# Kernel tuning notes

Hardware: AMD Instinct MI355X
Metric: run time of the kernel (lower is better)

## Reference

```python
import jax, jax.numpy as jnp
import numpy as np
from jax import lax

EPS = 1e-4
DN = ('NDHWC', 'DHWIO', 'NDHWC')


def _m(mask, dtype):
    return mask[..., None].astype(dtype)


def bn_relu(x, mask):
    # BatchNorm1d over active voxels only (training-mode batch stats, gamma=1, beta=0), then ReLU.
    m = _m(mask, x.dtype)
    n = jnp.sum(m)
    mean = jnp.sum(x * m, axis=(0, 1, 2, 3)) / n
    xc = (x - mean) * m  # re-mask: inactive voxels stay exactly zero
    var = jnp.sum(xc * xc, axis=(0, 1, 2, 3)) / n
    return jnp.maximum(xc * lax.rsqrt(var + EPS), 0.0)


def subm3(x, w, mask):
    # SubMConv3d k=3 pad=1: dense conv on zero-at-inactive input, output restricted to active sites.
    y = lax.conv_general_dilated(x, w, (1, 1, 1), 'SAME', dimension_numbers=DN)
    return y * _m(mask, x.dtype)


def down2(x, w):
    # SparseConv3d k=2 s=2: non-overlapping windows; inactive inputs are zero so dense strided conv matches.
    return lax.conv_general_dilated(x, w, (2, 2, 2), 'VALID', dimension_numbers=DN)


def pool_mask(mask):
    B, D, H, W = mask.shape
    return jnp.any(mask.reshape(B, D // 2, 2, H // 2, 2, W // 2, 2), axis=(2, 4, 6))


def up2(x, w, mask):
    # SparseInverseConv3d k=2 (indice_key inverse of the stride-2 conv): conv-transpose masked to original indices.
    y = jnp.einsum('bdhwc,ijkco->bdihjwko', x, w)
    B, Dc, _, Hc, _, Wc, _, Co = y.shape
    return y.reshape(B, 2 * Dc, 2 * Hc, 2 * Wc, Co) * _m(mask, x.dtype)


def resblock(x, mask, wa, wb, w_sc=None):
    # ResidualBlock: i_branch (identity or 1x1 Custom1x1Subm3d: feats @ W.T) + BN-ReLU-SubM-BN-ReLU-SubM.
    idb = x if w_sc is None else jnp.einsum('bdhwc,oc->bdhwo', x, w_sc)
    h = bn_relu(x, mask)
    h = subm3(h, wa, mask)
    h = bn_relu(h, mask)
    h = subm3(h, wb, mask)
    return h + idb


def unet_forward(x, mask, w_in, w_b1a, w_b1b, w_d1, w_b2a, w_b2b, w_d2,
                 w_b3a, w_b3b, w_u2, w_t2_sc, w_t2a, w_t2b, w_u1, w_t1_sc, w_t1a, w_t1b):
    mask2 = pool_mask(mask)
    mask3 = pool_mask(mask2)
    x0 = subm3(x, w_in, mask)                 # input_conv (subm1)
    x1 = resblock(x0, mask, w_b1a, w_b1b)     # level-1 block (32->32)
    d1 = down2(bn_relu(x1, mask), w_d1)       # BN-ReLU + stride-2 conv 32->64
    x2 = resblock(d1, mask2, w_b2a, w_b2b)    # level-2 block (64->64)
    d2 = down2(bn_relu(x2, mask2), w_d2)      # 64->96
    x3 = resblock(d2, mask3, w_b3a, w_b3b)    # bottom level (96->96)
    u2 = up2(bn_relu(x3, mask3), w_u2, mask2)  # BN-ReLU + inverse conv 96->64
    t2 = resblock(jnp.concatenate([x2, u2], -1), mask2, w_t2a, w_t2b, w_t2_sc)  # tail 128->64
    u1 = up2(bn_relu(t2, mask2), w_u1, mask)   # 64->32
    t1 = resblock(jnp.concatenate([x1, u1], -1), mask, w_t1a, w_t1b, w_t1_sc)   # tail 64->32
    return bn_relu(t1, mask)                   # output_layer: BN + ReLU


def setup_inputs() -> dict:
    key = jax.random.key(0)
    ks = jax.random.split(key, 20)
    B, D = 1, 48
    Cin, C1, C2, C3 = 6, 32, 64, 96
    mask = jax.random.uniform(ks[0], (B, D, D, D)) < 0.12
    x = jax.random.normal(ks[1], (B, D, D, D, Cin), jnp.float32) * mask[..., None]

    def w(k, shape):
        fan = float(np.prod(shape[:-1]))
        return (jax.random.normal(k, shape, jnp.float32) / np.sqrt(fan)).astype(jnp.float32)

    return {
        'x': x, 'mask': mask,
        'w_in': w(ks[2], (3, 3, 3, Cin, C1)),
        'w_b1a': w(ks[3], (3, 3, 3, C1, C1)), 'w_b1b': w(ks[4], (3, 3, 3, C1, C1)),
        'w_d1': w(ks[5], (2, 2, 2, C1, C2)),
        'w_b2a': w(ks[6], (3, 3, 3, C2, C2)), 'w_b2b': w(ks[7], (3, 3, 3, C2, C2)),
        'w_d2': w(ks[8], (2, 2, 2, C2, C3)),
        'w_b3a': w(ks[9], (3, 3, 3, C3, C3)), 'w_b3b': w(ks[10], (3, 3, 3, C3, C3)),
        'w_u2': w(ks[11], (2, 2, 2, C3, C2)),
        'w_t2_sc': w(ks[12], (C2, 2 * C2)),
        'w_t2a': w(ks[13], (3, 3, 3, 2 * C2, C2)), 'w_t2b': w(ks[14], (3, 3, 3, C2, C2)),
        'w_u1': w(ks[15], (2, 2, 2, C2, C1)),
        'w_t1_sc': w(ks[16], (C1, 2 * C1)),
        'w_t1a': w(ks[17], (3, 3, 3, 2 * C1, C1)), 'w_t1b': w(ks[18], (3, 3, 3, C1, C1)),
    }


def reference(x, mask, w_in, w_b1a, w_b1b, w_d1, w_b2a, w_b2b, w_d2,
              w_b3a, w_b3b, w_u2, w_t2_sc, w_t2a, w_t2b, w_u1, w_t1_sc, w_t1a, w_t1b):
    return unet_forward(x, mask, w_in, w_b1a, w_b1b, w_d1, w_b2a, w_b2b, w_d2,
                        w_b3a, w_b3b, w_u2, w_t2_sc, w_t2a, w_t2b, w_u1, w_t1_sc, w_t1a, w_t1b)
```

## Files before the change

### kernel.cpp

```cpp
#include <hip/hip_runtime.h>


typedef short bf16x8 __attribute__((ext_vector_type(8)));
typedef float f32x4 __attribute__((ext_vector_type(4)));
typedef unsigned short ushort_t;

constexpr int D1 = 48, DIM2 = 24, DIM3 = 12;
constexpr int N1 = D1 * D1 * D1;
constexpr int N2 = DIM2 * DIM2 * DIM2;
constexpr int N3 = DIM3 * DIM3 * DIM3;

constexpr size_t OFF_A      = 0;
constexpr size_t OFF_R1     = 3538944;
constexpr size_t OFF_CAT1   = 7077888;
constexpr size_t OFF_D1R    = 14155776;
constexpr size_t OFF_R3     = 15040512;
constexpr size_t OFF_CAT2   = 15925248;
constexpr size_t OFF_D2R    = 17694720;
constexpr size_t OFF_R4     = 17860608;
constexpr size_t OFF_X3R    = 18026496;
constexpr size_t OFF_BN1_32 = 18192384;
constexpr size_t OFF_BN1_64 = 19961920;
constexpr size_t OFF_BN2_64 = 23500928;
constexpr size_t OFF_BN2_128= 23943360;
constexpr size_t OFF_BN3_96 = 24828160;
constexpr size_t OFF_BFEND  = 24911168;
constexpr size_t OFF_WT     = 24911168;
constexpr size_t OFF_STATS  = 25634112;
constexpr size_t STATS_FLOATS = 15 * 2048 * 2;
constexpr size_t OFF_CNT    = OFF_STATS + STATS_FLOATS;
constexpr size_t OFF_L1     = OFF_CNT + 16;
constexpr size_t OFF_L2     = OFF_L1 + N1;
constexpr size_t OFF_L3     = OFF_L2 + N2;
constexpr size_t OFF_M1     = OFF_L3 + N3;
constexpr size_t OFF_M2     = OFF_M1 + N1 / 4;
constexpr size_t OFF_M3     = OFF_M2 + N2 / 4;

constexpr int WTS[16] = {0, 32768, 65536, 98304, 114688, 229376, 344064,
                         393216, 669696, 946176, 1175552, 1290240, 1347584,
                         1380352, 1429504, 1445888};

__device__ inline ushort_t f2bf(float f) {
  union { float f; unsigned u; } x; x.f = f;
  unsigned u = x.u + 0x7FFF + ((x.u >> 16) & 1);
  return (ushort_t)(u >> 16);
}

__global__ __launch_bounds__(256) void k_mask1(const float* __restrict__ x,
                                               unsigned char* __restrict__ m,
                                               int* __restrict__ list, int* __restrict__ cnt) {
  int v = blockIdx.x * 256 + threadIdx.x;
  if (v >= N1) return;
  const float* p = x + (size_t)v * 6;
  bool a = (p[0] != 0.f) || (p[1] != 0.f) || (p[2] != 0.f) ||
           (p[3] != 0.f) || (p[4] != 0.f) || (p[5] != 0.f);
  m[v] = a ? 1 : 0;
  if (a) { int pos = atomicAdd(cnt, 1); list[pos] = v; }
}

__global__ __launch_bounds__(256) void k_pool(const unsigned char* __restrict__ mf,
                                              unsigned char* __restrict__ mc,
                                              int* __restrict__ list, int* __restrict__ cnt, int DC) {
  int v = blockIdx.x * 256 + threadIdx.x;
  int n = DC * DC * DC;
  if (v >= n) return;
  int w = v % DC, h = (v / DC) % DC, d = v / (DC * DC);
  int DF = 2 * DC;
  bool a = false;
  for (int i = 0; i < 2; i++)
    for (int j = 0; j < 2; j++)
      for (int k = 0; k < 2; k++)
        a |= (mf[(size_t)(((2 * d + i) * DF + (2 * h + j)) * DF + (2 * w + k))] != 0);
  mc[v] = a ? 1 : 0;
  if (a) { int pos = atomicAdd(cnt, 1); list[pos] = v; }
}

struct WJobs {
  const float* src[15];
  int start[16];
  short cinr[15], cipad[15], cout[15], kk[15];
};

__global__ __launch_bounds__(256) void k_wprep(WJobs jb, ushort_t* __restrict__ wt, int total) {
  int gid = blockIdx.x * 256 + threadIdx.x;
  if (gid >= total) return;
  int j = 0;
#pragma unroll
  for (int jj = 0; jj < 15; jj++)
    if (gid >= jb.start[jj + 1]) j = jj + 1;
  int e = gid - jb.start[j];
  int CIP = jb.cipad[j], CO = jb.cout[j], CIR = jb.cinr[j], KKr = jb.kk[j];
  int ci = e % CIP;
  int co = (e / CIP) % CO;
  int k = e / (CIP * CO);
  float v = (k < KKr && ci < CIR) ? jb.src[j][((size_t)k * CIR + ci) * CO + co] : 0.f;
  wt[gid] = f2bf(v);
}

__global__ __launch_bounds__(256) void k_xprep(const float* __restrict__ x, ushort_t* __restrict__ xp) {
  int gid = blockIdx.x * 256 + threadIdx.x;
  if (gid >= (N1 + 4) * 8) return;
  int v = gid >> 3, c = (gid & 7) * 4;
  uint2 o = make_uint2(0u, 0u);
  if (v < N1) {
    ushort_t u[4];
#pragma unroll
    for (int j = 0; j < 4; j++) {
      int ci = c + j;
      float f = (ci < 6) ? x[(size_t)v * 6 + ci] : 0.f;
      u[j] = f2bf(f);
    }
    o.x = (unsigned)u[0] | ((unsigned)u[1] << 16);
    o.y = (unsigned)u[2] | ((unsigned)u[3] << 16);
  }
  *(uint2*)&xp[(size_t)v * 32 + c] = o;
}

template <int CIPAD, int COUT, int KK, bool UP>
__global__ __launch_bounds__(512, 2) void k_conv4(
    const ushort_t* __restrict__ in, const ushort_t* __restrict__ wt,
    float* __restrict__ out, int ostride, int ooff,
    const float* __restrict__ res, int rstride,
    double* __restrict__ st,
    const int* __restrict__ list, const int* __restrict__ cnt, int DD) {
  constexpr int KCH = CIPAD / 32;
  constexpr int UNITS = KK * KCH;
  constexpr int KPW = (UNITS + 7) / 8;
  __shared__ float red[8][8][64];
  __shared__ float fin[16][33];
  __shared__ int vidx[16];

  int n = cnt[0];
  int base = blockIdx.x * 16;
  if (base >= n) return;
  int t = threadIdx.x, wv = t >> 6, ln = t & 63;
  int fr = ln & 15, kg = ln >> 4;
  int coblk = blockIdx.y * 32;
  if (t < 16) vidx[t] = (base + t < n) ? list[base + t] : -1;

  int ai = base + fr;
  int av = (ai < n) ? list[ai] : -1;
  int vv = av < 0 ? 0 : av;
  int ad = vv / (DD * DD), ah = (vv / DD) % DD, aw = vv % DD;
  int pidx = 0, corner = 0;
  if (UP) {
    int DC = DD / 2;
    pidx = (((ad >> 1) * DC) + (ah >> 1)) * DC + (aw >> 1);
    corner = ((ad & 1) << 2) | ((ah & 1) << 1) | (aw & 1);
  }
  const int GDI = UP ? (DD >> 1) : ((KK == 8) ? 2 * DD : DD);
  const int SENT = GDI * GDI * GDI;

  f32x4 acc0 = (f32x4){0.f, 0.f, 0.f, 0.f};
  f32x4 acc1 = (f32x4){0.f, 0.f, 0.f, 0.f};

  bf16x8 aR[KPW], b0R[KPW], b1R[KPW];
#pragma unroll
  for (int i = 0; i < KPW; i++) {
    int u = wv + i * 8;
    int k = u / KCH, c = u - k * KCH;
    int kc = (k < KK) ? k : KK - 1;
    int nix;
    if (UP) {
      nix = (av >= 0 && corner == kc) ? pidx : SENT;
    } else if (KK == 27) {
      int kd = kc / 9 - 1, kh = (kc / 3) % 3 - 1, kw = kc % 3 - 1;
      int nd = ad + kd, nh = ah + kh, nw = aw + kw;
      bool inb = (av >= 0) && (unsigned)nd < (unsigned)DD &&
                 (unsigned)nh < (unsigned)DD && (unsigned)nw < (unsigned)DD;
      nix = inb ? (nd * DD + nh) * DD + nw : SENT;
    } else {
      nix = (av >= 0) ? ((2 * ad + ((kc >> 2) & 1)) * GDI + (2 * ah + ((kc >> 1) & 1))) * GDI +
                        (2 * aw + (kc & 1))
                      : SENT;
    }
    aR[i] = *(const bf16x8*)(in + (size_t)nix * CIPAD + c * 32 + kg * 8);
    const ushort_t* wb = wt + ((size_t)(k * COUT + coblk + fr)) * CIPAD + c * 32 + kg * 8;
    b0R[i] = *(const bf16x8*)wb;
    b1R[i] = *(const bf16x8*)(wb + (size_t)16 * CIPAD);
  }
#pragma unroll
  for (int i = 0; i < KPW; i++) {
    acc0 = __builtin_amdgcn_mfma_f32_16x16x32_bf16(aR[i], b0R[i], acc0, 0, 0, 0);
    acc1 = __builtin_amdgcn_mfma_f32_16x16x32_bf16(aR[i], b1R[i], acc1, 0, 0, 0);
  }

#pragma unroll
  for (int r = 0; r < 4; r++) {
    red[wv][r][ln] = acc0[r];
    red[wv][4 + r][ln] = acc1[r];
  }
  __syncthreads();
  {
    int e = t >> 6, l = t & 63;
    float s = 0.f;
#pragma unroll
    for (int w = 0; w < 8; w++) s += red[w][e][l];
    int f = e >> 2, r = e & 3;
    int fr2 = l & 15, kg2 = l >> 4;
    int slot = kg2 * 4 + r;
    int co = f * 16 + fr2;
    int v = vidx[slot];
    float val = 0.f;
    if (v >= 0) {
      int gco = coblk + co;
      val = s;
      if (res) val += res[(size_t)v * rstride + gco];
      out[(size_t)v * ostride + ooff + gco] = val;
    }
    fin[slot][co] = val;
  }
  __syncthreads();
  if (t < 32) {
    float sm = 0.f, sq = 0.f;
#pragma unroll
    for (int p = 0; p < 16; p++) {
      float x = fin[p][t];
      sm += x; sq += x * x;
    }
    double* sr = st + (size_t)(blockIdx.x & 7) * 256;
    atomicAdd(&sr[coblk + t], (double)sm);
    atomicAdd(&sr[128 + coblk + t], (double)sq);
  }
}

template <int C>
__global__ __launch_bounds__(256) void k_bnapply2(
    const float* __restrict__ x, int xstr,
    const double* __restrict__ sA, const double* __restrict__ sB, int csplit,
    const int* __restrict__ list, const int* __restrict__ cnt,
    ushort_t* __restrict__ out) {
  __shared__ float mu_s[C], inv_s[C];
  int n = cnt[0];
  int t = threadIdx.x;
  if (t < C) {
    const double* s = (t < csplit) ? (sA + t) : (sB + (t - csplit));
    double sm = 0.0, sq = 0.0;
#pragma unroll
    for (int r = 0; r < 8; r++) { sm += s[r * 256]; sq += s[r * 256 + 128]; }
    double mu = sm / n;
    double var = sq / n - mu * mu;
    mu_s[t] = (float)mu;
    inv_s[t] = rsqrtf((float)fmax(var, 0.0) + 1e-4f);
  }
  __syncthreads();
  int total = n * (C / 4);
  for (int gid = blockIdx.x * 256 + t; gid < total; gid += gridDim.x * 256) {
    int i = gid / (C / 4);
    int c = (gid % (C / 4)) * 4;
    int v = list[i];
    float4 xv = *(const float4*)&x[(size_t)v * xstr + c];
    float xa[4] = {xv.x, xv.y, xv.z, xv.w};
    ushort_t u[4];
#pragma unroll
    for (int j = 0; j < 4; j++)
      u[j] = f2bf(fmaxf((xa[j] - mu_s[c + j]) * inv_s[c + j], 0.f));
    uint2 o; o.x = (unsigned)u[0] | ((unsigned)u[1] << 16);
    o.y = (unsigned)u[2] | ((unsigned)u[3] << 16);
    *(uint2*)&out[(size_t)v * C + c] = o;
  }
}

__global__ __launch_bounds__(256) void k_bnout(const float* __restrict__ x,
                                               const unsigned char* __restrict__ m,
                                               const double* __restrict__ s,
                                               const int* __restrict__ cnt,
                                               float* __restrict__ out) {
  __shared__ float mu_s[32], inv_s[32];
  int t = threadIdx.x;
  int n = cnt[0];
  if (t < 32) {
    double sm = 0.0, sq = 0.0;
#pragma unroll
    for (int r = 0; r < 8; r++) { sm += s[r * 256 + t]; sq += s[r * 256 + 128 + t]; }
    double mu = sm / n;
    double var = sq / n - mu * mu;
    mu_s[t] = (float)mu;
    inv_s[t] = rsqrtf((float)fmax(var, 0.0) + 1e-4f);
  }
  __syncthreads();
  int gid = blockIdx.x * 256 + t;
  if (gid >= N1 * 8) return;
  int v = gid / 8;
  int c = (gid % 8) * 4;
  float4 o = make_float4(0.f, 0.f, 0.f, 0.f);
  if (m[v]) {
    float4 xv = *(const float4*)&x[(size_t)v * 32 + c];
    o.x = fmaxf((xv.x - mu_s[c + 0]) * inv_s[c + 0], 0.f);
    o.y = fmaxf((xv.y - mu_s[c + 1]) * inv_s[c + 1], 0.f);
    o.z = fmaxf((xv.z - mu_s[c + 2]) * inv_s[c + 2], 0.f);
    o.w = fmaxf((xv.w - mu_s[c + 3]) * inv_s[c + 3], 0.f);
  }
  *(float4*)&out[(size_t)v * 32 + c] = o;
}

template <int CI, int CO>
__global__ __launch_bounds__(256) void k_sc(const float* __restrict__ in,
                                            const float* __restrict__ wsc,
                                            float* __restrict__ out,
                                            const int* __restrict__ list,
                                            const int* __restrict__ cnt) {
  int n = cnt[0];
  long total = (long)n * CO;
  for (long gid = (long)blockIdx.x * 256 + threadIdx.x; gid < total; gid += (long)gridDim.x * 256) {
    int i = (int)(gid / CO), o = (int)(gid % CO);
    int v = list[i];
    const float4* xr = (const float4*)(in + (size_t)v * CI);
    const float4* wr = (const float4*)(wsc + (size_t)o * CI);
    float a = 0.f;
    for (int c = 0; c < CI / 4; c++) {
      float4 x4 = xr[c], w4 = wr[c];
      a += x4.x * w4.x + x4.y * w4.y + x4.z * w4.z + x4.w * w4.w;
    }
    out[(size_t)v * CO + o] = a;
  }
}

extern "C" void kernel_launch(void* const* d_in, const int* in_sizes, int n_in,
                              void* d_out, int out_size, void* d_ws, size_t ws_size,
                              hipStream_t stream) {
  float* W = (float*)d_ws;
  const float* x = (const float*)d_in[0];

  float* A    = W + OFF_A;
  float* R1   = W + OFF_R1;
  float* CAT1 = W + OFF_CAT1;
  float* D1R  = W + OFF_D1R;
  float* R3   = W + OFF_R3;
  float* CAT2 = W + OFF_CAT2;
  float* D2R  = W + OFF_D2R;
  float* R4   = W + OFF_R4;
  float* X3R  = W + OFF_X3R;
  ushort_t* XP     = (ushort_t*)(W + OFF_CAT1);
  ushort_t* BN1_32 = (ushort_t*)(W + OFF_BN1_32);
  ushort_t* BN1_64 = (ushort_t*)(W + OFF_BN1_64);
  ushort_t* BN2_64 = (ushort_t*)(W + OFF_BN2_64);
  ushort_t* BN2_128= (ushort_t*)(W + OFF_BN2_128);
  ushort_t* BN3_96 = (ushort_t*)(W + OFF_BN3_96);
  ushort_t* WT  = (ushort_t*)(W + OFF_WT);
  double* S0 = (double*)(W + OFF_STATS);
  int* CNT = (int*)(W + OFF_CNT);
  int* L1 = (int*)(W + OFF_L1);
  int* L2 = (int*)(W + OFF_L2);
  int* L3 = (int*)(W + OFF_L3);
  unsigned char* M1 = (unsigned char*)(W + OFF_M1);
  unsigned char* M2 = (unsigned char*)(W + OFF_M2);
  unsigned char* M3 = (unsigned char*)(W + OFF_M3);

  auto S = [&](int i) { return S0 + (size_t)i * 2048; };

  hipMemsetAsync(W + OFF_STATS, 0, (STATS_FLOATS + 16) * 4, stream);
  hipMemsetAsync(W + OFF_BN1_32, 0, (OFF_BFEND - OFF_BN1_32) * 4, stream);

  k_mask1<<<N1 / 256, 256, 0, stream>>>(x, M1, L1, CNT + 0);
  k_pool<<<N2 / 256, 256, 0, stream>>>(M1, M2, L2, CNT + 1, DIM2);
  k_pool<<<(N3 + 255) / 256, 256, 0, stream>>>(M2, M3, L3, CNT + 2, DIM3);

  WJobs jb;
  const int srcIdx[15] = {2, 3, 4, 5, 6, 7, 8, 9, 10, 13, 14, 17, 18, 11, 15};
  const short cinr[15]  = {6, 32, 32, 32, 64, 64, 64, 96, 96, 128, 64, 64, 32, 96, 64};
  const short cipad[15] = {32, 32, 32, 32, 64, 64, 64, 96, 96, 128, 64, 64, 32, 96, 64};
  const short couts[15] = {32, 32, 32, 64, 64, 64, 96, 96, 96, 64, 64, 32, 32, 64, 32};
  const short kkr[15]   = {27, 27, 27, 8, 27, 27, 8, 27, 27, 27, 27, 27, 27, 8, 8};
  for (int j = 0; j < 15; j++) {
    jb.src[j] = (const float*)d_in[srcIdx[j]];
    jb.cinr[j] = cinr[j]; jb.cipad[j] = cipad[j]; jb.cout[j] = couts[j];
    jb.kk[j] = kkr[j];
    jb.start[j] = WTS[j];
  }
  jb.start[15] = WTS[15];
  k_wprep<<<(WTS[15] + 255) / 256, 256, 0, stream>>>(jb, WT, WTS[15]);
  k_xprep<<<((N1 + 4) * 8 + 255) / 256, 256, 0, stream>>>(x, XP);

  const int GT1 = 1024;
  const int GT2 = 640;
  const int GT3 = 108;
  const int BNG = 512;

  k_conv4<32, 32, 27, false><<<dim3(GT1, 1), 512, 0, stream>>>(
      XP, WT + WTS[0], A, 32, 0, nullptr, 0, S(0), L1, CNT + 0, D1);
  k_bnapply2<32><<<BNG, 256, 0, stream>>>(A, 32, S(0), S(0), 32, L1, CNT + 0, BN1_32);
  k_conv4<32, 32, 27, false><<<dim3(GT1, 1), 512, 0, stream>>>(
      BN1_32, WT + WTS[1], R1, 32, 0, nullptr, 0, S(1), L1, CNT + 0, D1);
  k_bnapply2<32><<<BNG, 256, 0, stream>>>(R1, 32, S(1), S(1), 32, L1, CNT + 0, BN1_32);
  k_conv4<32, 32, 27, false><<<dim3(GT1, 1), 512, 0, stream>>>(
      BN1_32, WT + WTS[2], CAT1, 64, 0, A, 32, S(2), L1, CNT + 0, D1);
  k_bnapply2<32><<<BNG, 256, 0, stream>>>(CAT1, 64, S(2), S(2), 32, L1, CNT + 0, BN1_32);
  k_conv4<32, 64, 8, false><<<dim3(GT2, 2), 512, 0, stream>>>(
      BN1_32, WT + WTS[3], D1R, 64, 0, nullptr, 0, S(3), L2, CNT + 1, DIM2);

  k_bnapply2<64><<<BNG, 256, 0, stream>>>(D1R, 64, S(3), S(3), 64, L2, CNT + 1, BN2_64);
  k_conv4<64, 64, 27, false><<<dim3(GT2, 2), 512, 0, stream>>>(
      BN2_64, WT + WTS[4], R3, 64, 0, nullptr, 0, S(4), L2, CNT + 1, DIM2);
  k_bnapply2<64><<<BNG, 256, 0, stream>>>(R3, 64, S(4), S(4), 64, L2, CNT + 1, BN2_64);
  k_conv4<64, 64, 27, false><<<dim3(GT2, 2), 512, 0, stream>>>(
      BN2_64, WT + WTS[5], CAT2, 128, 0, D1R, 64, S(5), L2, CNT + 1, DIM2);
  k_bnapply2<64><<<BNG, 256, 0, stream>>>(CAT2, 128, S(5), S(5), 64, L2, CNT + 1, BN2_64);
  k_conv4<64, 96, 8, false><<<dim3(GT3, 3), 512, 0, stream>>>(
      BN2_64, WT + WTS[6], D2R, 96, 0, nullptr, 0, S(6), L3, CNT + 2, DIM3);

  k_bnapply2<96><<<BNG, 256, 0, stream>>>(D2R, 96, S(6), S(6), 96, L3, CNT + 2, BN3_96);
  k_conv4<96, 96, 27, false><<<dim3(GT3, 3), 512, 0, stream>>>(
      BN3_96, WT + WTS[7], R4, 96, 0, nullptr, 0, S(7), L3, CNT + 2, DIM3);
  k_bnapply2<96><<<BNG, 256, 0, stream>>>(R4, 96, S(7), S(7), 96, L3, CNT + 2, BN3_96);
  k_conv4<96, 96, 27, false><<<dim3(GT3, 3), 512, 0, stream>>>(
      BN3_96, WT + WTS[8], X3R, 96, 0, D2R, 96, S(8), L3, CNT + 2, DIM3);
  k_bnapply2<96><<<BNG, 256, 0, stream>>>(X3R, 96, S(8), S(8), 96, L3, CNT + 2, BN3_96);
  k_conv4<96, 64, 8, true><<<dim3(GT2, 2), 512, 0, stream>>>(
      BN3_96, WT + WTS[13], CAT2, 128, 64, nullptr, 0, S(9), L2, CNT + 1, DIM2);

  k_bnapply2<128><<<BNG, 256, 0, stream>>>(CAT2, 128, S(5), S(9), 64, L2, CNT + 1, BN2_128);
  k_conv4<128, 64, 27, false><<<dim3(GT2, 2), 512, 0, stream>>>(
      BN2_128, WT + WTS[9], R3, 64, 0, nullptr, 0, S(10), L2, CNT + 1, DIM2);
  k_bnapply2<64><<<BNG, 256, 0, stream>>>(R3, 64, S(10), S(10), 64, L2, CNT + 1, BN2_64);
  k_sc<128, 64><<<512, 256, 0, stream>>>(CAT2, (const float*)d_in[12], D1R, L2, CNT + 1);
  k_conv4<64, 64, 27, false><<<dim3(GT2, 2), 512, 0, stream>>>(
      BN2_64, WT + WTS[10], R3, 64, 0, D1R, 64, S(11), L2, CNT + 1, DIM2);
  k_bnapply2<64><<<BNG, 256, 0, stream>>>(R3, 64, S(11), S(11), 64, L2, CNT + 1, BN2_64);
  k_conv4<64, 32, 8, true><<<dim3(GT1, 1), 512, 0, stream>>>(
      BN2_64, WT + WTS[14], CAT1, 64, 32, nullptr, 0, S(12), L1, CNT + 0, D1);

  k_bnapply2<64><<<BNG, 256, 0, stream>>>(CAT1, 64, S(2), S(12), 32, L1, CNT + 0, BN1_64);
  k_conv4<64, 32, 27, false><<<dim3(GT1, 1), 512, 0, stream>>>(
      BN1_64, WT + WTS[11], R1, 32, 0, nullptr, 0, S(13), L1, CNT + 0, D1);
  k_bnapply2<32><<<BNG, 256, 0, stream>>>(R1, 32, S(13), S(13), 32, L1, CNT + 0, BN1_32);
  k_sc<64, 32><<<512, 256, 0, stream>>>(CAT1, (const float*)d_in[16], A, L1, CNT + 0);
  k_conv4<32, 32, 27, false><<<dim3(GT1, 1), 512, 0, stream>>>(
      BN1_32, WT + WTS[12], A, 32, 0, A, 32, S(14), L1, CNT + 0, D1);
  k_bnout<<<N1 * 8 / 256, 256, 0, stream>>>(A, M1, S(14), CNT + 0, (float*)d_out);
}
```

Before: 409.8 us.

## Process 32 voxels per conv block with per-wave tap split and double-buffered loads

The gather-conv kernel now handles 32 active voxels per block instead of 16. Its 8 waves are split into 2 voxel groups times 4 kernel-tap slices. Each wave walks its taps with a two-register-set ping-pong, so the next tap's gathered activations and weights load while the current tap's MFMAs run. Grid sizes are halved to match, and the cross-wave reduction now sums four partials per voxel group instead of eight. The aim is to amortise per-block overhead, the reduction and the stats atomics over more voxels and to overlap load latency with compute. In exchange, each wave holds more registers and the grid has fewer blocks to fill the GPU, especially at the coarsest level.

```diff
diff --git a/kernel.cpp b/kernel.cpp
--- a/kernel.cpp
+++ b/kernel.cpp
@@ -117,28 +117,28 @@
 }
 
 template <int CIPAD, int COUT, int KK, bool UP>
-__global__ __launch_bounds__(512, 2) void k_conv4(
+__global__ __launch_bounds__(512, 2) void k_conv6(
     const ushort_t* __restrict__ in, const ushort_t* __restrict__ wt,
     float* __restrict__ out, int ostride, int ooff,
     const float* __restrict__ res, int rstride,
     double* __restrict__ st,
     const int* __restrict__ list, const int* __restrict__ cnt, int DD) {
   constexpr int KCH = CIPAD / 32;
-  constexpr int UNITS = KK * KCH;
-  constexpr int KPW = (UNITS + 7) / 8;
+  constexpr int TPS = (KK + 3) / 4;
   __shared__ float red[8][8][64];
-  __shared__ float fin[16][33];
-  __shared__ int vidx[16];
+  __shared__ float fin[32][33];
+  __shared__ int vidx[32];
 
   int n = cnt[0];
-  int base = blockIdx.x * 16;
+  int base = blockIdx.x * 32;
   if (base >= n) return;
   int t = threadIdx.x, wv = t >> 6, ln = t & 63;
+  int vg = wv & 1, ks = wv >> 1;
   int fr = ln & 15, kg = ln >> 4;
   int coblk = blockIdx.y * 32;
-  if (t < 16) vidx[t] = (base + t < n) ? list[base + t] : -1;
-
-  int ai = base + fr;
+  if (t < 32) vidx[t] = (base + t < n) ? list[base + t] : -1;
+
+  int ai = base + vg * 16 + fr;
   int av = (ai < n) ? list[ai] : -1;
   int vv = av < 0 ? 0 : av;
   int ad = vv / (DD * DD), ah = (vv / DD) % DD, aw = vv % DD;
@@ -151,39 +151,59 @@
   const int GDI = UP ? (DD >> 1) : ((KK == 8) ? 2 * DD : DD);
   const int SENT = GDI * GDI * GDI;
 
-  f32x4 acc0 = (f32x4){0.f, 0.f, 0.f, 0.f};
-  f32x4 acc1 = (f32x4){0.f, 0.f, 0.f, 0.f};
-
-  bf16x8 aR[KPW], b0R[KPW], b1R[KPW];
-#pragma unroll
-  for (int i = 0; i < KPW; i++) {
-    int u = wv + i * 8;
-    int k = u / KCH, c = u - k * KCH;
+  int k0 = ks * TPS;
+
+  auto nixOf = [&](int k) -> int {
     int kc = (k < KK) ? k : KK - 1;
-    int nix;
     if (UP) {
-      nix = (av >= 0 && corner == kc) ? pidx : SENT;
+      return (av >= 0 && corner == kc) ? pidx : SENT;
     } else if (KK == 27) {
       int kd = kc / 9 - 1, kh = (kc / 3) % 3 - 1, kw = kc % 3 - 1;
       int nd = ad + kd, nh = ah + kh, nw = aw + kw;
       bool inb = (av >= 0) && (unsigned)nd < (unsigned)DD &&
                  (unsigned)nh < (unsigned)DD && (unsigned)nw < (unsigned)DD;
-      nix = inb ? (nd * DD + nh) * DD + nw : SENT;
+      return inb ? (nd * DD + nh) * DD + nw : SENT;
     } else {
-      nix = (av >= 0) ? ((2 * ad + ((kc >> 2) & 1)) * GDI + (2 * ah + ((kc >> 1) & 1))) * GDI +
-                        (2 * aw + (kc & 1))
-                      : SENT;
+      return (av >= 0) ? ((2 * ad + ((kc >> 2) & 1)) * GDI + (2 * ah + ((kc >> 1) & 1))) * GDI +
+                             (2 * aw + (kc & 1))
+                       : SENT;
     }
-    aR[i] = *(const bf16x8*)(in + (size_t)nix * CIPAD + c * 32 + kg * 8);
-    const ushort_t* wb = wt + ((size_t)(k * COUT + coblk + fr)) * CIPAD + c * 32 + kg * 8;
-    b0R[i] = *(const bf16x8*)wb;
-    b1R[i] = *(const bf16x8*)(wb + (size_t)16 * CIPAD);
-  }
-#pragma unroll
-  for (int i = 0; i < KPW; i++) {
-    acc0 = __builtin_amdgcn_mfma_f32_16x16x32_bf16(aR[i], b0R[i], acc0, 0, 0, 0);
-    acc1 = __builtin_amdgcn_mfma_f32_16x16x32_bf16(aR[i], b1R[i], acc1, 0, 0, 0);
-  }
+  };
+
+  f32x4 acc0 = (f32x4){0.f, 0.f, 0.f, 0.f};
+  f32x4 acc1 = (f32x4){0.f, 0.f, 0.f, 0.f};
+
+  bf16x8 aX[KCH], bX[2 * KCH], aY[KCH], bY[2 * KCH];
+
+#define LOADSET(AR, BR, J)                                                         \
+  {                                                                                \
+    int kk_ = k0 + (J);                                                            \
+    int nix_ = nixOf(kk_);                                                         \
+    const ushort_t* ap_ = in + (size_t)nix_ * CIPAD + kg * 8;                      \
+    _Pragma("unroll") for (int c = 0; c < KCH; c++)                                \
+        AR[c] = *(const bf16x8*)(ap_ + c * 32);                                    \
+    const ushort_t* wb_ = wt + ((size_t)(kk_ * COUT + coblk + fr)) * CIPAD + kg * 8; \
+    _Pragma("unroll") for (int c = 0; c < KCH; c++) {                              \
+      BR[c] = *(const bf16x8*)(wb_ + c * 32);                                      \
+      BR[KCH + c] = *(const bf16x8*)(wb_ + (size_t)16 * CIPAD + c * 32);           \
+    }                                                                              \
+  }
+#define MFMASET(AR, BR)                                                            \
+  _Pragma("unroll") for (int c = 0; c < KCH; c++) {                                \
+    acc0 = __builtin_amdgcn_mfma_f32_16x16x32_bf16(AR[c], BR[c], acc0, 0, 0, 0);   \
+    acc1 = __builtin_amdgcn_mfma_f32_16x16x32_bf16(AR[c], BR[KCH + c], acc1, 0, 0, 0); \
+  }
+
+  LOADSET(aX, bX, 0);
+#pragma unroll
+  for (int j = 0; j < TPS; j += 2) {
+    if (j + 1 < TPS) LOADSET(aY, bY, j + 1);
+    MFMASET(aX, bX);
+    if (j + 2 < TPS) LOADSET(aX, bX, j + 2);
+    if (j + 1 < TPS) MFMASET(aY, bY);
+  }
+#undef LOADSET
+#undef MFMASET
 
 #pragma unroll
   for (int r = 0; r < 4; r++) {
@@ -191,14 +211,15 @@
     red[wv][4 + r][ln] = acc1[r];
   }
   __syncthreads();
-  {
-    int e = t >> 6, l = t & 63;
-    float s = 0.f;
-#pragma unroll
-    for (int w = 0; w < 8; w++) s += red[w][e][l];
-    int f = e >> 2, r = e & 3;
-    int fr2 = l & 15, kg2 = l >> 4;
-    int slot = kg2 * 4 + r;
+#pragma unroll
+  for (int e0 = 0; e0 < 2; e0++) {
+    int e = t + e0 * 512;
+    int ln2 = e & 63, r = (e >> 6) & 3, f = (e >> 8) & 1, vg2 = e >> 9;
+    int ei = f * 4 + r;
+    float s = red[vg2][ei][ln2] + red[2 + vg2][ei][ln2] +
+              red[4 + vg2][ei][ln2] + red[6 + vg2][ei][ln2];
+    int fr2 = ln2 & 15, kg2 = ln2 >> 4;
+    int slot = vg2 * 16 + kg2 * 4 + r;
     int co = f * 16 + fr2;
     int v = vidx[slot];
     float val = 0.f;
@@ -214,7 +235,7 @@
   if (t < 32) {
     float sm = 0.f, sq = 0.f;
 #pragma unroll
-    for (int p = 0; p < 16; p++) {
+    for (int p = 0; p < 32; p++) {
       float x = fin[p][t];
       sm += x; sq += x * x;
     }
@@ -372,60 +393,58 @@
   k_wprep<<<(WTS[15] + 255) / 256, 256, 0, stream>>>(jb, WT, WTS[15]);
   k_xprep<<<((N1 + 4) * 8 + 255) / 256, 256, 0, stream>>>(x, XP);
 
-  const int GT1 = 1024;
-  const int GT2 = 640;
-  const int GT3 = 108;
+  const int GB1 = 512, GB2 = 320, GB3 = 54;
   const int BNG = 512;
 
-  k_conv4<32, 32, 27, false><<<dim3(GT1, 1), 512, 0, stream>>>(
+  k_conv6<32, 32, 27, false><<<dim3(GB1, 1), 512, 0, stream>>>(
       XP, WT + WTS[0], A, 32, 0, nullptr, 0, S(0), L1, CNT + 0, D1);
   k_bnapply2<32><<<BNG, 256, 0, stream>>>(A, 32, S(0), S(0), 32, L1, CNT + 0, BN1_32);
-  k_conv4<32, 32, 27, false><<<dim3(GT1, 1), 512, 0, stream>>>(
+  k_conv6<32, 32, 27, false><<<dim3(GB1, 1), 512, 0, stream>>>(
       BN1_32, WT + WTS[1], R1, 32, 0, nullptr, 0, S(1), L1, CNT + 0, D1);
   k_bnapply2<32><<<BNG, 256, 0, stream>>>(R1, 32, S(1), S(1), 32, L1, CNT + 0, BN1_32);
-  k_conv4<32, 32, 27, false><<<dim3(GT1, 1), 512, 0, stream>>>(
+  k_conv6<32, 32, 27, false><<<dim3(GB1, 1), 512, 0, stream>>>(
       BN1_32, WT + WTS[2], CAT1, 64, 0, A, 32, S(2), L1, CNT + 0, D1);
   k_bnapply2<32><<<BNG, 256, 0, stream>>>(CAT1, 64, S(2), S(2), 32, L1, CNT + 0, BN1_32);
-  k_conv4<32, 64, 8, false><<<dim3(GT2, 2), 512, 0, stream>>>(
+  k_conv6<32, 64, 8, false><<<dim3(GB2, 2), 512, 0, stream>>>(
       BN1_32, WT + WTS[3], D1R, 64, 0, nullptr, 0, S(3), L2, CNT + 1, DIM2);
 
   k_bnapply2<64><<<BNG, 256, 0, stream>>>(D1R, 64, S(3), S(3), 64, L2, CNT + 1, BN2_64);
-  k_conv4<64, 64, 27, false><<<dim3(GT2, 2), 512, 0, stream>>>(
+  k_conv6<64, 64, 27, false><<<dim3(GB2, 2), 512, 0, stream>>>(
       BN2_64, WT + WTS[4], R3, 64, 0, nullptr, 0, S(4), L2, CNT + 1, DIM2);
   k_bnapply2<64><<<BNG, 256, 0, stream>>>(R3, 64, S(4), S(4), 64, L2, CNT + 1, BN2_64);
-  k_conv4<64, 64, 27, false><<<dim3(GT2, 2), 512, 0, stream>>>(
+  k_conv6<64, 64, 27, false><<<dim3(GB2, 2), 512, 0, stream>>>(
       BN2_64, WT + WTS[5], CAT2, 128, 0, D1R, 64, S(5), L2, CNT + 1, DIM2);
   k_bnapply2<64><<<BNG, 256, 0, stream>>>(CAT2, 128, S(5), S(5), 64, L2, CNT + 1, BN2_64);
-  k_conv4<64, 96, 8, false><<<dim3(GT3, 3), 512, 0, stream>>>(
+  k_conv6<64, 96, 8, false><<<dim3(GB3, 3), 512, 0, stream>>>(
       BN2_64, WT + WTS[6], D2R, 96, 0, nullptr, 0, S(6), L3, CNT + 2, DIM3);
 
   k_bnapply2<96><<<BNG, 256, 0, stream>>>(D2R, 96, S(6), S(6), 96, L3, CNT + 2, BN3_96);
-  k_conv4<96, 96, 27, false><<<dim3(GT3, 3), 512, 0, stream>>>(
+  k_conv6<96, 96, 27, false><<<dim3(GB3, 3), 512, 0, stream>>>(
       BN3_96, WT + WTS[7], R4, 96, 0, nullptr, 0, S(7), L3, CNT + 2, DIM3);
   k_bnapply2<96><<<BNG, 256, 0, stream>>>(R4, 96, S(7), S(7), 96, L3, CNT + 2, BN3_96);
-  k_conv4<96, 96, 27, false><<<dim3(GT3, 3), 512, 0, stream>>>(
+  k_conv6<96, 96, 27, false><<<dim3(GB3, 3), 512, 0, stream>>>(
       BN3_96, WT + WTS[8], X3R, 96, 0, D2R, 96, S(8), L3, CNT + 2, DIM3);
   k_bnapply2<96><<<BNG, 256, 0, stream>>>(X3R, 96, S(8), S(8), 96, L3, CNT + 2, BN3_96);
-  k_conv4<96, 64, 8, true><<<dim3(GT2, 2), 512, 0, stream>>>(
+  k_conv6<96, 64, 8, true><<<dim3(GB2, 2), 512, 0, stream>>>(
       BN3_96, WT + WTS[13], CAT2, 128, 64, nullptr, 0, S(9), L2, CNT + 1, DIM2);
 
   k_bnapply2<128><<<BNG, 256, 0, stream>>>(CAT2, 128, S(5), S(9), 64, L2, CNT + 1, BN2_128);
-  k_conv4<128, 64, 27, false><<<dim3(GT2, 2), 512, 0, stream>>>(
+  k_conv6<128, 64, 27, false><<<dim3(GB2, 2), 512, 0, stream>>>(
       BN2_128, WT + WTS[9], R3, 64, 0, nullptr, 0, S(10), L2, CNT + 1, DIM2);
   k_bnapply2<64><<<BNG, 256, 0, stream>>>(R3, 64, S(10), S(10), 64, L2, CNT + 1, BN2_64);
   k_sc<128, 64><<<512, 256, 0, stream>>>(CAT2, (const float*)d_in[12], D1R, L2, CNT + 1);
-  k_conv4<64, 64, 27, false><<<dim3(GT2, 2), 512, 0, stream>>>(
+  k_conv6<64, 64, 27, false><<<dim3(GB2, 2), 512, 0, stream>>>(
       BN2_64, WT + WTS[10], R3, 64, 0, D1R, 64, S(11), L2, CNT + 1, DIM2);
   k_bnapply2<64><<<BNG, 256, 0, stream>>>(R3, 64, S(11), S(11), 64, L2, CNT + 1, BN2_64);
-  k_conv4<64, 32, 8, true><<<dim3(GT1, 1), 512, 0, stream>>>(
+  k_conv6<64, 32, 8, true><<<dim3(GB1, 1), 512, 0, stream>>>(
       BN2_64, WT + WTS[14], CAT1, 64, 32, nullptr, 0, S(12), L1, CNT + 0, D1);
 
   k_bnapply2<64><<<BNG, 256, 0, stream>>>(CAT1, 64, S(2), S(12), 32, L1, CNT + 0, BN1_64);
-  k_conv4<64, 32, 27, false><<<dim3(GT1, 1), 512, 0, stream>>>(
+  k_conv6<64, 32, 27, false><<<dim3(GB1, 1), 512, 0, stream>>>(
       BN1_64, WT + WTS[11], R1, 32, 0, nullptr, 0, S(13), L1, CNT + 0, D1);
   k_bnapply2<32><<<BNG, 256, 0, stream>>>(R1, 32, S(13), S(13), 32, L1, CNT + 0, BN1_32);
   k_sc<64, 32><<<512, 256, 0, stream>>>(CAT1, (const float*)d_in[16], A, L1, CNT + 0);
-  k_conv4<32, 32, 27, false><<<dim3(GT1, 1), 512, 0, stream>>>(
+  k_conv6<32, 32, 27, false><<<dim3(GB1, 1), 512, 0, stream>>>(
       BN1_32, WT + WTS[12], A, 32, 0, A, 32, S(14), L1, CNT + 0, D1);
   k_bnout<<<N1 * 8 / 256, 256, 0, stream>>>(A, M1, S(14), CNT + 0, (float*)d_out);
 }
```

New measurement: 418.8 us. +2.2%, slower.
